# Kernel tuning notes

Hardware: AMD Instinct MI355X
Metric: run time of the kernel (lower is better)

The kernel has to match this reference:

```python
import jax, jax.numpy as jnp
import numpy as np

DIM = 128; PDIM = 32; WS = 16; HEADS = 4; NBLK = 2

def gelu(x):
    return jax.nn.gelu(x, approximate=False)  # torch default GELU (erf)

def conv2d(x, w, b=None, pad=0, groups=1):
    y = jax.lax.conv_general_dilated(x, w, (1, 1), [(pad, pad), (pad, pad)],
                                     feature_group_count=groups,
                                     dimension_numbers=('NCHW', 'OIHW', 'NCHW'))
    if b is not None:
        y = y + b[None, :, None, None]
    return y

def layernorm_cf(x, w, b, eps=1e-6):
    # channels_first LayerNorm over C per (b,h,w)
    m = x.mean(axis=1, keepdims=True)
    v = ((x - m) ** 2).mean(axis=1, keepdims=True)
    return (x - m) / jnp.sqrt(v + eps) * w[None, :, None, None] + b[None, :, None, None]

def conv_ffn(x, w1, b1, dw, dwb, w2, b2):
    y = gelu(conv2d(x, w1, b1, 0))
    y = gelu(conv2d(y, dw, dwb, 1, groups=y.shape[1])) + y
    return conv2d(y, w2, b2, 0)

def conv_attention(x, lk, pw1, pb1, pw2, pb2):
    # ConvolutionalAttention (training branch math, non-inplace)
    B, C, H, W = x.shape
    x1, x2 = x[:, :PDIM], x[:, PDIM:]
    # dwc_proj: global avg pool -> 1x1 -> GELU -> 1x1 (pure matmuls on pooled vec)
    v = x1.mean(axis=(2, 3))                              # [B, PDIM]
    h = gelu(v @ pw1[:, :, 0, 0].T + pb1)                 # [B, PDIM//2]
    dk = (h @ pw2[:, :, 0, 0].T + pb2).reshape(B * PDIM, 1, 3, 3)
    # per-sample dynamic depthwise conv via groups = B*PDIM
    dyn = conv2d(x1.reshape(1, B * PDIM, H, W), dk, None, 1,
                 groups=B * PDIM).reshape(B, PDIM, H, W)
    x1 = conv2d(x1, lk, None, lk.shape[-1] // 2) + dyn
    return jnp.concatenate([x1, x2], axis=1)

def window_attention(x, qkv_w, qkv_b, out_w, out_b, table):
    B, C, H, W = x.shape  # H,W divisible by WS -> pad_to_win is a no-op
    hd, wd = H // WS, W // WS
    c = C // HEADS
    qkv = conv2d(x, qkv_w, qkv_b, 0)                      # [B, 3C, H, W]
    qkv = qkv.reshape(B, 3, HEADS, c, hd, WS, wd, WS)
    qkv = qkv.transpose(1, 0, 4, 6, 2, 5, 7, 3).reshape(3, B * hd * wd, HEADS, WS * WS, c)
    q, k, v = qkv[0], qkv[1], qkv[2]
    S = WS * WS
    idx = jnp.arange(S); qh = idx // WS; qw = idx % WS
    rel = (qh[None, :] - qh[:, None] + WS - 1) * (2 * WS - 1) + (qw[None, :] - qw[:, None] + WS - 1)
    bias = table[:, rel]                                  # [HEADS, S, S]
    scores = jnp.einsum('nhqc,nhkc->nhqk', q, k) * (c ** -0.5) + bias[None]
    attn = jax.nn.softmax(scores, axis=-1)
    o = jnp.einsum('nhqk,nhkc->nhqc', attn, v)
    o = o.reshape(B, hd, wd, HEADS, WS, WS, c).transpose(0, 3, 6, 1, 4, 2, 5).reshape(B, C, H, W)
    return conv2d(o, out_w, out_b, 0)

def forward(x, plk_filter, ln_proj_w, ln_proj_b, proj_w1, proj_b1, proj_dw, proj_dwb,
            proj_w2, proj_b2, ln_attn_w, ln_attn_b, qkv_w, qkv_b, attn_out_w, attn_out_b,
            rpe_table, ffn_w1, ffn_b1, ffn_dw, ffn_dwb, ffn_w2, ffn_b2,
            pk_w1, pk_b1, pk_w2, pk_b2, pk_aggr_w, pk_aggr_b,
            ln_out_w, ln_out_b, co_w, co_b):
    skip = x
    x = layernorm_cf(x, ln_proj_w, ln_proj_b)
    x = conv_ffn(x, proj_w1, proj_b1, proj_dw, proj_dwb, proj_w2, proj_b2)
    x = x + window_attention(layernorm_cf(x, ln_attn_w, ln_attn_b),
                             qkv_w, qkv_b, attn_out_w, attn_out_b, rpe_table)
    for i in range(NBLK):
        y = conv_ffn(x, ffn_w1[i], ffn_b1[i], ffn_dw[i], ffn_dwb[i], ffn_w2[i], ffn_b2[i])
        y = conv_attention(y, plk_filter, pk_w1[i], pk_b1[i], pk_w2[i], pk_b2[i])
        y = conv2d(y, pk_aggr_w[i], pk_aggr_b[i], 0)
        x = x + y
    x = conv2d(layernorm_cf(x, ln_out_w, ln_out_b), co_w, co_b, 1)
    return x + skip

def setup_inputs() -> dict:
    key = jax.random.key(0)
    ks = iter(jax.random.split(key, 64))
    def rn(shape, s=0.02):
        return jax.random.normal(next(ks), shape, jnp.float32) * s
    d = DIM; e = 2 * d
    return dict(
        x=jax.random.normal(next(ks), (4, d, 192, 192), jnp.float32),
        plk_filter=rn((PDIM, PDIM, 13, 13), 0.05),
        ln_proj_w=jnp.ones((d,), jnp.float32), ln_proj_b=jnp.zeros((d,), jnp.float32),
        proj_w1=rn((e, d, 1, 1)), proj_b1=rn((e,)),
        proj_dw=rn((e, 1, 3, 3), 0.1), proj_dwb=rn((e,)),
        proj_w2=rn((d, e, 1, 1)), proj_b2=rn((d,)),
        ln_attn_w=jnp.ones((d,), jnp.float32), ln_attn_b=jnp.zeros((d,), jnp.float32),
        qkv_w=rn((3 * d, d, 1, 1)), qkv_b=rn((3 * d,)),
        attn_out_w=rn((d, d, 1, 1)), attn_out_b=rn((d,)),
        rpe_table=rn((HEADS, (2 * WS - 1) ** 2), 0.001),
        ffn_w1=rn((NBLK, e, d, 1, 1)), ffn_b1=rn((NBLK, e)),
        ffn_dw=rn((NBLK, e, 1, 3, 3), 0.1), ffn_dwb=rn((NBLK, e)),
        ffn_w2=rn((NBLK, d, e, 1, 1)), ffn_b2=rn((NBLK, d)),
        pk_w1=rn((NBLK, PDIM // 2, PDIM, 1, 1)), pk_b1=rn((NBLK, PDIM // 2)),
        pk_w2=rn((NBLK, PDIM * 9, PDIM // 2, 1, 1), 0.01), pk_b2=rn((NBLK, PDIM * 9), 0.01),
        pk_aggr_w=rn((NBLK, d, d, 1, 1)), pk_aggr_b=rn((NBLK, d)),
        ln_out_w=jnp.ones((d,), jnp.float32), ln_out_b=jnp.zeros((d,), jnp.float32),
        co_w=rn((d, d, 3, 3), 0.05), co_b=rn((d,)),
    )

def reference(x, plk_filter, ln_proj_w, ln_proj_b, proj_w1, proj_b1, proj_dw, proj_dwb,
              proj_w2, proj_b2, ln_attn_w, ln_attn_b, qkv_w, qkv_b, attn_out_w, attn_out_b,
              rpe_table, ffn_w1, ffn_b1, ffn_dw, ffn_dwb, ffn_w2, ffn_b2,
              pk_w1, pk_b1, pk_w2, pk_b2, pk_aggr_w, pk_aggr_b,
              ln_out_w, ln_out_b, co_w, co_b):
    return forward(x, plk_filter, ln_proj_w, ln_proj_b, proj_w1, proj_b1, proj_dw, proj_dwb,
                   proj_w2, proj_b2, ln_attn_w, ln_attn_b, qkv_w, qkv_b, attn_out_w, attn_out_b,
                   rpe_table, ffn_w1, ffn_b1, ffn_dw, ffn_dwb, ffn_w2, ffn_b2,
                   pk_w1, pk_b1, pk_w2, pk_b2, pk_aggr_w, pk_aggr_b,
                   ln_out_w, ln_out_b, co_w, co_b)
```

## Files before the change

kernel.cpp:

```cpp
#include <hip/hip_runtime.h>
#include <cmath>

#define HWD 192
#define PIX (HWD*HWD)
#define BB  4
#define CCH 128

using short8 = __attribute__((ext_vector_type(8))) short;
using f32x4  = __attribute__((ext_vector_type(4))) float;

__device__ __forceinline__ float gelu_f(float x) {
    return 0.5f * x * (1.0f + erff(x * 0.70710678118654752f));
}
__device__ __forceinline__ unsigned short f2bf(float f) {
    unsigned int u = __float_as_uint(f);
    u += 0x7fff + ((u >> 16) & 1);
    return (unsigned short)(u >> 16);
}
__device__ __forceinline__ float bf2f(unsigned short s) {
    return __uint_as_float((unsigned int)s << 16);
}
__device__ __forceinline__ unsigned pack2bf(float a, float b) {
    return (unsigned)f2bf(a) | ((unsigned)f2bf(b) << 16);
}

__global__ __launch_bounds__(256) void ln_t_kernel(const float* __restrict__ in,
        const float* __restrict__ w, const float* __restrict__ b,
        unsigned short* __restrict__ outT)
{
    int t = blockIdx.x * 256 + threadIdx.x;
    int bi = t / PIX;
    int p  = t - bi*PIX;
    const float* base = in + (size_t)bi * CCH * PIX + p;
    float v[CCH];
    float s = 0.f;
    #pragma unroll
    for (int c=0;c<CCH;++c) { v[c] = base[(size_t)c*PIX]; s += v[c]; }
    float m = s * (1.f/128.f);
    float q = 0.f;
    #pragma unroll
    for (int c=0;c<CCH;++c) { float d = v[c]-m; q += d*d; }
    float iv = rsqrtf(q*(1.f/128.f) + 1e-6f);
    unsigned short* ob = outT + ((size_t)bi * PIX + p) * 128;
    #pragma unroll
    for (int qq=0; qq<16; ++qq) {
        unsigned short e[8];
        #pragma unroll
        for (int j=0;j<8;++j) {
            int c = qq*8 + j;
            e[j] = f2bf((v[c]-m)*iv*w[c] + b[c]);
        }
        *(uint4*)&ob[qq*8] = *(uint4*)e;
    }
}

__global__ __launch_bounds__(256) void t32_kernel(const unsigned short* __restrict__ in,
    unsigned short* __restrict__ outT)
{
    int t = blockIdx.x * 256 + threadIdx.x;
    int bi = t / PIX;
    int p  = t - bi*PIX;
    const unsigned short* base = in + (size_t)bi * CCH * PIX + p;
    unsigned short e[32];
    #pragma unroll
    for (int c=0;c<32;++c) e[c] = base[(size_t)c*PIX];
    unsigned short* ob = outT + ((size_t)bi * PIX + p) * 32;
    #pragma unroll
    for (int q=0;q<4;++q) *(uint4*)&ob[q*8] = *(uint4*)&e[q*8];
}

template<typename TIN, bool TRANSIN, bool DOGELU, bool DORES, bool OBF>
__global__ __launch_bounds__(256) void conv1x1_mfma_kernel(
    const TIN* __restrict__ in,
    const unsigned short* __restrict__ wq,
    const float* __restrict__ bias,
    const float* __restrict__ res,
    void* __restrict__ outv,
    int Cin)
{
    constexpr int CIP = 72;
    __shared__ unsigned short XL[128*CIP];
    const int Cout = gridDim.y * 128;
    const int px0 = blockIdx.x * 128;
    const int co0 = blockIdx.y * 128;
    const size_t bi = blockIdx.z;
    in  += bi * (size_t)Cin * PIX;
    if (DORES) res += bi * (size_t)Cout * PIX;
    float* outf = (float*)outv + bi * (size_t)Cout * PIX;
    unsigned short* outb = (unsigned short*)outv + bi * (size_t)Cout * PIX;
    const int tid = threadIdx.x;
    const int lane = tid & 63, wid = tid >> 6;
    const int wco = (wid >> 1) * 64;
    const int wpx = (wid & 1) * 64;
    const int l15 = lane & 15, l4 = lane >> 4;

    f32x4 acc[4][4];
    #pragma unroll
    for (int i=0;i<4;++i)
        #pragma unroll
        for (int j=0;j<4;++j) acc[i][j] = (f32x4){0.f,0.f,0.f,0.f};

    for (int k0 = 0; k0 < Cin; k0 += 64) {
        __syncthreads();
        if constexpr (TRANSIN) {
            #pragma unroll
            for (int it = 0; it < 4; ++it) {
                int idx = tid + it*256;
                int q = idx & 7, px = idx >> 3;
                const uint4 v = *(const uint4*)((const unsigned short*)in
                                + ((size_t)(px0 + px))*128 + k0 + q*8);
                *(uint4*)&XL[px*CIP + q*8] = v;
            }
        } else {
            #pragma unroll
            for (int it = 0; it < 2; ++it) {
                int idx = tid + it*256;
                int c2  = idx & 31;
                int s   = idx >> 5;
                const TIN* g0 = in + (size_t)(k0 + c2*2    )*PIX + px0 + s*8;
                const TIN* g1 = in + (size_t)(k0 + c2*2 + 1)*PIX + px0 + s*8;
                unsigned short a8[8], b8[8];
                if constexpr (sizeof(TIN) == 2) {
                    *(uint4*)a8 = *(const uint4*)g0;
                    *(uint4*)b8 = *(const uint4*)g1;
                } else {
                    const float4 f0 = *(const float4*)g0;
                    const float4 f1 = *(const float4*)(g0+4);
                    const float4 f2 = *(const float4*)g1;
                    const float4 f3 = *(const float4*)(g1+4);
                    a8[0]=f2bf(f0.x); a8[1]=f2bf(f0.y); a8[2]=f2bf(f0.z); a8[3]=f2bf(f0.w);
                    a8[4]=f2bf(f1.x); a8[5]=f2bf(f1.y); a8[6]=f2bf(f1.z); a8[7]=f2bf(f1.w);
                    b8[0]=f2bf(f2.x); b8[1]=f2bf(f2.y); b8[2]=f2bf(f2.z); b8[3]=f2bf(f2.w);
                    b8[4]=f2bf(f3.x); b8[5]=f2bf(f3.y); b8[6]=f2bf(f3.z); b8[7]=f2bf(f3.w);
                }
                #pragma unroll
                for (int j=0;j<8;++j) {
                    unsigned pk = (unsigned)a8[j] | ((unsigned)b8[j] << 16);
                    *(unsigned*)&XL[(s*8+j)*CIP + c2*2] = pk;
                }
            }
        }
        __syncthreads();
        #pragma unroll
        for (int ks = 0; ks < 2; ++ks) {
            short8 a[4];
            #pragma unroll
            for (int mt=0; mt<4; ++mt) {
                int co = co0 + wco + mt*16 + l15;
                a[mt] = *(const short8*)(wq + (size_t)co*Cin + k0 + ks*32 + l4*8);
            }
            #pragma unroll
            for (int nt=0; nt<4; ++nt) {
                const short8 b = *(const short8*)&XL[(wpx + nt*16 + l15)*CIP + ks*32 + l4*8];
                #pragma unroll
                for (int mt=0; mt<4; ++mt)
                    acc[mt][nt] = __builtin_amdgcn_mfma_f32_16x16x32_bf16(a[mt], b, acc[mt][nt], 0, 0, 0);
            }
        }
    }
    #pragma unroll
    for (int mt=0; mt<4; ++mt) {
        #pragma unroll
        for (int r=0; r<4; ++r) {
            int co = co0 + wco + mt*16 + l4*4 + r;
            float bs = bias[co];
            #pragma unroll
            for (int nt=0; nt<4; ++nt) {
                int px = px0 + wpx + nt*16 + l15;
                float v = acc[mt][nt][r] + bs;
                if (DOGELU) v = gelu_f(v);
                size_t o = (size_t)co*PIX + px;
                if (DORES) v += res[o];
                if (OBF) outb[o] = f2bf(v);
                else     outf[o] = v;
            }
        }
    }
}

__global__ __launch_bounds__(256) void conv3x3_mfma_kernel(
    const unsigned short* __restrict__ inT,
    const unsigned short* __restrict__ wq,
    const float* __restrict__ bias, const float* __restrict__ skip,
    float* __restrict__ out)
{
    constexpr int CIP = 72;
    __shared__ unsigned short XL[4*66*CIP];
    const int x0 = blockIdx.x * 64;
    const int y0 = blockIdx.y * 2;
    const int bi = blockIdx.z;
    const int tid = threadIdx.x;
    const int lane = tid & 63, wid = tid >> 6;
    const int wco = (wid >> 1) * 64;
    const int wrow = wid & 1;
    const int l15 = lane & 15, l4 = lane >> 4;
    const unsigned short* inb = inT + (size_t)bi * PIX * 128;

    f32x4 acc[4][4];
    #pragma unroll
    for (int i=0;i<4;++i)
        #pragma unroll
        for (int j=0;j<4;++j) acc[i][j] = (f32x4){0.f,0.f,0.f,0.f};

    for (int ci0 = 0; ci0 < 128; ci0 += 64) {
        __syncthreads();
        #pragma unroll
        for (int it = 0; it < 9; ++it) {
            int idx = tid + it*256;
            if (idx < 2112) {
                int P = idx >> 3;
                int q = idx & 7;
                int row = P / 66;
                int x = P - row*66;
                int gy = y0 - 1 + row, gx = x0 - 1 + x;
                uint4 v = {0u,0u,0u,0u};
                if ((unsigned)gy < (unsigned)HWD && (unsigned)gx < (unsigned)HWD)
                    v = *(const uint4*)&inb[((size_t)gy*HWD + gx)*128 + ci0 + q*8];
                *(uint4*)&XL[P*CIP + q*8] = v;
            }
        }
        __syncthreads();
        #pragma unroll
        for (int dy=0; dy<3; ++dy) {
            #pragma unroll
            for (int dx=0; dx<3; ++dx) {
                const int rl = wrow + dy;
                #pragma unroll
                for (int ks=0; ks<2; ++ks) {
                    short8 a[4];
                    #pragma unroll
                    for (int mt=0; mt<4; ++mt) {
                        int co = wco + mt*16 + l15;
                        a[mt] = *(const short8*)(wq + ((size_t)co*9 + dy*3+dx)*128 + ci0 + ks*32 + l4*8);
                    }
                    #pragma unroll
                    for (int nt=0; nt<4; ++nt) {
                        const int xl = nt*16 + l15 + dx;
                        const short8 b = *(const short8*)&XL[(rl*66 + xl)*CIP + ks*32 + l4*8];
                        #pragma unroll
                        for (int mt=0; mt<4; ++mt)
                            acc[mt][nt] = __builtin_amdgcn_mfma_f32_16x16x32_bf16(a[mt], b, acc[mt][nt], 0, 0, 0);
                    }
                }
            }
        }
    }
    const int gy = y0 + wrow;
    #pragma unroll
    for (int mt=0; mt<4; ++mt) {
        #pragma unroll
        for (int r=0; r<4; ++r) {
            int co = wco + mt*16 + l4*4 + r;
            float bs = bias[co];
            #pragma unroll
            for (int nt=0; nt<4; ++nt) {
                int gx = x0 + nt*16 + l15;
                size_t o = ((size_t)bi*CCH + co)*PIX + (size_t)gy*HWD + gx;
                out[o] = acc[mt][nt][r] + bs + skip[o];
            }
        }
    }
}

__global__ __launch_bounds__(256) void conv13_mfma_kernel(
    const unsigned short* __restrict__ YT,
    const unsigned short* __restrict__ wq,
    const float* __restrict__ dk,
    unsigned short* __restrict__ outL)
{
    __shared__ unsigned short XL[16*76*32];
    const int x0 = blockIdx.x * 64;
    const int y0 = blockIdx.y * 4;
    const int bi = blockIdx.z;
    const int tid = threadIdx.x;
    const int lane = tid & 63, wr = tid >> 6;
    const int l15 = lane & 15, l4 = lane >> 4;
    const unsigned short* inT = YT + (size_t)bi * PIX * 32;

    #pragma unroll 1
    for (int it = 0; it < 19; ++it) {
        int idx = tid + it*256;
        int P = idx >> 2;
        int q = idx & 3;
        int row = P / 76;
        int x   = P - row*76;
        int gy = y0 - 6 + row, gx = x0 - 6 + x;
        uint4 v = {0u,0u,0u,0u};
        if ((unsigned)gy < (unsigned)HWD && (unsigned)gx < (unsigned)HWD)
            v = *(const uint4*)&inT[((size_t)gy*HWD + gx)*32 + q*8];
        *(uint4*)&XL[P*32 + ((q*8) ^ ((P&3)<<3))] = v;
    }
    __syncthreads();

    f32x4 acc[2][4];
    #pragma unroll
    for (int i=0;i<2;++i)
        #pragma unroll
        for (int j=0;j<4;++j) acc[i][j] = (f32x4){0.f,0.f,0.f,0.f};

    #pragma unroll 1
    for (int dy=0; dy<13; ++dy) {
        const unsigned short* wrow = wq + (size_t)dy*13*1024;
        #pragma unroll
        for (int dx=0; dx<13; ++dx) {
            const short8 a0 = *(const short8*)(wrow + dx*1024 + l15*32 + l4*8);
            const short8 a1 = *(const short8*)(wrow + dx*1024 + (16+l15)*32 + l4*8);
            #pragma unroll
            for (int nt=0; nt<4; ++nt) {
                const int P = (wr + dy)*76 + nt*16 + l15 + dx;
                const short8 b = *(const short8*)&XL[P*32 + ((l4*8) ^ ((P&3)<<3))];
                acc[0][nt] = __builtin_amdgcn_mfma_f32_16x16x32_bf16(a0, b, acc[0][nt], 0, 0, 0);
                acc[1][nt] = __builtin_amdgcn_mfma_f32_16x16x32_bf16(a1, b, acc[1][nt], 0, 0, 0);
            }
        }
    }
    const int gy = y0 + wr;
    #pragma unroll
    for (int mt=0; mt<2; ++mt) {
        #pragma unroll
        for (int r=0; r<4; ++r) {
            const int co = mt*16 + l4*4 + r;
            const float* dkk = dk + (bi*32 + co)*9;
            float k0=dkk[0],k1=dkk[1],k2=dkk[2],k3=dkk[3],k4=dkk[4],
                  k5=dkk[5],k6=dkk[6],k7=dkk[7],k8=dkk[8];
            #pragma unroll
            for (int nt=0; nt<4; ++nt) {
                const int px = nt*16 + l15;
                float dsum = 0.f;
                #pragma unroll
                for (int e=0; e<9; ++e) {
                    int ey = e/3, ex = e - ey*3;
                    int P = (wr+5+ey)*76 + px+5+ex;
                    float pv = bf2f(XL[P*32 + (co ^ ((P&3)<<3))]);
                    float kk = (e==0?k0:e==1?k1:e==2?k2:e==3?k3:e==4?k4:e==5?k5:e==6?k6:e==7?k7:k8);
                    dsum += pv * kk;
                }
                float v = acc[mt][nt][r] + dsum;
                outL[((size_t)bi*CCH + co)*PIX + (size_t)gy*HWD + x0 + px] = f2bf(v);
            }
        }
    }
}

__global__ __launch_bounds__(256) void dw3x3_bf_kernel(const unsigned short* __restrict__ in,
    const float* __restrict__ w, const float* __restrict__ b,
    unsigned short* __restrict__ out)
{
    int t = blockIdx.x*256 + threadIdx.x;
    int pc = t / (PIX/4);
    int p4 = (t - pc*(PIX/4)) * 4;
    int c = pc & 255;
    int y = p4 / HWD, x0 = p4 - y*HWD;
    const unsigned short* ib = in + (size_t)pc * PIX;
    float wk[9];
    #pragma unroll
    for (int e=0;e<9;++e) wk[e] = w[c*9+e];
    float bc = b[c];
    float a0=bc,a1=bc,a2=bc,a3=bc;
    #pragma unroll
    for (int ky=0;ky<3;++ky) {
        int yy = y + ky - 1;
        if ((unsigned)yy < (unsigned)HWD) {
            const unsigned short* row = ib + (size_t)yy*HWD;
            float v[6];
            #pragma unroll
            for (int d=0;d<6;++d) {
                int xx = x0 + d - 1;
                v[d] = ((unsigned)xx < (unsigned)HWD) ? bf2f(row[xx]) : 0.f;
            }
            a0 += v[0]*wk[ky*3+0] + v[1]*wk[ky*3+1] + v[2]*wk[ky*3+2];
            a1 += v[1]*wk[ky*3+0] + v[2]*wk[ky*3+1] + v[3]*wk[ky*3+2];
            a2 += v[2]*wk[ky*3+0] + v[3]*wk[ky*3+1] + v[4]*wk[ky*3+2];
            a3 += v[3]*wk[ky*3+0] + v[4]*wk[ky*3+1] + v[5]*wk[ky*3+2];
        }
    }
    const unsigned short* cen = ib + (size_t)y*HWD + x0;
    unsigned short r0 = f2bf(gelu_f(a0) + bf2f(cen[0]));
    unsigned short r1 = f2bf(gelu_f(a1) + bf2f(cen[1]));
    unsigned short r2 = f2bf(gelu_f(a2) + bf2f(cen[2]));
    unsigned short r3 = f2bf(gelu_f(a3) + bf2f(cen[3]));
    uint2 pk;
    pk.x = (unsigned)r0 | ((unsigned)r1 << 16);
    pk.y = (unsigned)r2 | ((unsigned)r3 << 16);
    *(uint2*)(out + (size_t)pc*PIX + p4) = pk;
}

__global__ __launch_bounds__(256) void attn_mfma_kernel(
    const unsigned short* __restrict__ qkv,
    const float* __restrict__ table,
    unsigned short* __restrict__ o)
{
    __shared__ unsigned short KL[256*44];
    __shared__ unsigned short VL[32*264];
    __shared__ unsigned short PL[4*16*40];
    __shared__ float BT[961];
    __shared__ unsigned short OL[64*33];
    const int win = blockIdx.x, head = blockIdx.y;
    const int bi2 = blockIdx.z;
    const int wy = win/12, wx = win - wy*12;
    qkv += (size_t)bi2 * 384 * PIX;
    o   += (size_t)bi2 * CCH * PIX;
    const unsigned short* qb = qkv + (size_t)(head*32) * PIX;
    const unsigned short* kb = qkv + (size_t)(128 + head*32) * PIX;
    const unsigned short* vb = qkv + (size_t)(256 + head*32) * PIX;
    const int tid = threadIdx.x;

    #pragma unroll
    for (int it = 0; it < 4; ++it) {
        int idx = tid + it*256;
        int c = idx & 31, seg = idx >> 5;
        int k0 = seg*8;
        int sp = ((wy<<4) + (k0>>4))*HWD + (wx<<4) + (k0&15);
        *(uint4*)&VL[c*264 + k0] = *(const uint4*)&vb[(size_t)c*PIX + sp];
    }
    #pragma unroll
    for (int it = 0; it < 4; ++it) {
        int idx = tid + it*256;
        int c = idx & 31, seg = idx >> 5;
        int k0 = seg*8;
        int sp = ((wy<<4) + (k0>>4))*HWD + (wx<<4) + (k0&15);
        unsigned short e[8];
        *(uint4*)e = *(const uint4*)&kb[(size_t)c*PIX + sp];
        #pragma unroll
        for (int j=0;j<8;++j) KL[(k0+j)*44 + c] = e[j];
    }
    for (int i = tid; i < 961; i += 256) BT[i] = table[head*961 + i];
    __syncthreads();

    const int lane = tid & 63, w = tid >> 6;
    const int l15 = lane & 15, l4 = lane >> 4;
    const float scale = 0.17677669529663687f;
    unsigned short* PLw = &PL[w*16*40];

    #pragma unroll 1
    for (int qc = 0; qc < 4; ++qc) {
        const int qi = qc*64 + w*16 + l15;
        const int iy = qi >> 4, ix = qi & 15;
        const int spq = ((wy<<4) + iy)*HWD + (wx<<4) + ix;

        short8 qf;
        #pragma unroll
        for (int j=0;j<8;++j) qf[j] = (short)qb[(size_t)(l4*8+j)*PIX + spq];

        f32x4 s[16];
        #pragma unroll
        for (int nt=0; nt<16; ++nt) {
            const short8 a = *(const short8*)&KL[(nt*16 + l15)*44 + l4*8];
            s[nt] = __builtin_amdgcn_mfma_f32_16x16x32_bf16(a, qf, (f32x4){0.f,0.f,0.f,0.f}, 0, 0, 0);
        }

        float m = -1e30f;
        #pragma unroll
        for (int nt=0; nt<16; ++nt) {
            #pragma unroll
            for (int r=0; r<4; ++r) {
                int k = nt*16 + l4*4 + r;
                float bv = BT[((k>>4) - iy + 15)*31 + ((k&15) - ix + 15)];
                float v = s[nt][r]*scale + bv;
                s[nt][r] = v;
                m = fmaxf(m, v);
            }
        }
        m = fmaxf(m, __shfl_xor(m, 16, 64));
        m = fmaxf(m, __shfl_xor(m, 32, 64));
        float l = 0.f;
        #pragma unroll
        for (int nt=0; nt<16; ++nt) {
            #pragma unroll
            for (int r=0; r<4; ++r) {
                float p = __expf(s[nt][r] - m);
                s[nt][r] = p;
                l += p;
            }
        }
        l += __shfl_xor(l, 16, 64);
        l += __shfl_xor(l, 32, 64);

        f32x4 o0 = (f32x4){0.f,0.f,0.f,0.f}, o1 = (f32x4){0.f,0.f,0.f,0.f};
        #pragma unroll
        for (int kt=0; kt<8; ++kt) {
            #pragma unroll
            for (int h=0; h<2; ++h) {
                int nt = kt*2 + h;
                *(unsigned*)&PLw[l15*40 + h*16 + l4*4]     = pack2bf(s[nt][0], s[nt][1]);
                *(unsigned*)&PLw[l15*40 + h*16 + l4*4 + 2] = pack2bf(s[nt][2], s[nt][3]);
            }
            const short8 pa = *(const short8*)&PLw[l15*40 + l4*8];
            const short8 v0 = *(const short8*)&VL[l15*264 + kt*32 + l4*8];
            const short8 v1 = *(const short8*)&VL[(16+l15)*264 + kt*32 + l4*8];
            o0 = __builtin_amdgcn_mfma_f32_16x16x32_bf16(pa, v0, o0, 0, 0, 0);
            o1 = __builtin_amdgcn_mfma_f32_16x16x32_bf16(pa, v1, o1, 0, 0, 0);
        }

        #pragma unroll
        for (int r=0; r<4; ++r) {
            float lr = __shfl(l, l4*4 + r, 64);
            float inv = 1.f / lr;
            OL[(w*16 + l4*4 + r)*33 + l15]      = f2bf(o0[r]*inv);
            OL[(w*16 + l4*4 + r)*33 + 16 + l15] = f2bf(o1[r]*inv);
        }
        __syncthreads();

        const int d = tid >> 3, seg = tid & 7;
        const int q0l = seg*8;
        const int qi0 = qc*64 + q0l;
        const int sp0 = ((wy<<4) + (qi0>>4))*HWD + (wx<<4) + (qi0 & 15);
        unsigned short tmp[8];
        #pragma unroll
        for (int j=0;j<8;++j) tmp[j] = OL[(q0l+j)*33 + d];
        *(uint4*)&o[(size_t)(head*32 + d)*PIX + sp0] = *(uint4*)tmp;
        __syncthreads();
    }
}

__global__ __launch_bounds__(256) void meanpool_kernel(const unsigned short* __restrict__ in,
    float* __restrict__ v)
{
    int bc = blockIdx.x;
    int bi = bc >> 5, c = bc & 31;
    const unsigned short* base = in + ((size_t)bi*CCH + c) * PIX;
    float s = 0.f;
    for (int i = threadIdx.x; i < PIX/4; i += 256) {
        const uint2 t4 = ((const uint2*)base)[i];
        s += bf2f((unsigned short)(t4.x & 0xffff)) + bf2f((unsigned short)(t4.x >> 16))
           + bf2f((unsigned short)(t4.y & 0xffff)) + bf2f((unsigned short)(t4.y >> 16));
    }
    #pragma unroll
    for (int off=32; off>0; off>>=1) s += __shfl_down(s, off, 64);
    __shared__ float red[4];
    if ((threadIdx.x & 63) == 0) red[threadIdx.x >> 6] = s;
    __syncthreads();
    if (threadIdx.x == 0) v[bc] = (red[0]+red[1]+red[2]+red[3]) * (1.f/PIX);
}

__global__ __launch_bounds__(256) void mlp_kernel(const float* __restrict__ v,
    const float* __restrict__ pw1, const float* __restrict__ pb1,
    const float* __restrict__ pw2, const float* __restrict__ pb2,
    float* __restrict__ dk)
{
    __shared__ float h[64];
    int tid = threadIdx.x;
    if (tid < 64) {
        int bi = tid >> 4, m = tid & 15;
        float s = pb1[m];
        for (int c=0;c<32;++c) s += v[bi*32+c]*pw1[m*32+c];
        h[tid] = gelu_f(s);
    }
    __syncthreads();
    for (int idx = tid; idx < BB*288; idx += 256) {
        int bi = idx / 288, j = idx - bi*288;
        float s = pb2[j];
        for (int m=0;m<16;++m) s += h[bi*16+m]*pw2[j*16+m];
        dk[idx] = s;
    }
}

__global__ __launch_bounds__(256) void wcast_kernel(const float* __restrict__ w,
    unsigned short* __restrict__ wq, int n)
{
    int idx = blockIdx.x*256 + threadIdx.x;
    if (idx < n) wq[idx] = f2bf(w[idx]);
}

__global__ __launch_bounds__(256) void w3cast_kernel(const float* __restrict__ w,
    unsigned short* __restrict__ wq)
{
    int idx = blockIdx.x*256 + threadIdx.x;
    if (idx >= 128*128*9) return;
    int co = idx / (128*9);
    int rem = idx - co*128*9;
    int ci = rem / 9;
    int tap = rem - ci*9;
    wq[((size_t)co*9 + tap)*128 + ci] = f2bf(w[idx]);
}

__global__ __launch_bounds__(256) void w13cast_kernel(const float* __restrict__ w,
    unsigned short* __restrict__ wq)
{
    int idx = blockIdx.x*256 + threadIdx.x;
    if (idx >= 32*32*169) return;
    int co = idx / (32*169);
    int rem = idx - co*32*169;
    int ci = rem / 169;
    int tap = rem - ci*169;
    wq[((size_t)tap*32 + co)*32 + ci] = f2bf(w[idx]);
}

extern "C" void kernel_launch(void* const* d_in, const int* in_sizes, int n_in,
                              void* d_out, int out_size, void* d_ws, size_t ws_size,
                              hipStream_t stream) {
    (void)in_sizes; (void)n_in; (void)out_size;
    const float* x_in      = (const float*)d_in[0];
    const float* plk       = (const float*)d_in[1];
    const float* ln_proj_w = (const float*)d_in[2];
    const float* ln_proj_b = (const float*)d_in[3];
    const float* proj_w1   = (const float*)d_in[4];
    const float* proj_b1   = (const float*)d_in[5];
    const float* proj_dw   = (const float*)d_in[6];
    const float* proj_dwb  = (const float*)d_in[7];
    const float* proj_w2   = (const float*)d_in[8];
    const float* proj_b2   = (const float*)d_in[9];
    const float* ln_attn_w = (const float*)d_in[10];
    const float* ln_attn_b = (const float*)d_in[11];
    const float* qkv_w     = (const float*)d_in[12];
    const float* qkv_b     = (const float*)d_in[13];
    const float* attn_ow   = (const float*)d_in[14];
    const float* attn_ob   = (const float*)d_in[15];
    const float* rpe       = (const float*)d_in[16];
    const float* ffn_w1    = (const float*)d_in[17];
    const float* ffn_b1    = (const float*)d_in[18];
    const float* ffn_dw    = (const float*)d_in[19];
    const float* ffn_dwb   = (const float*)d_in[20];
    const float* ffn_w2    = (const float*)d_in[21];
    const float* ffn_b2    = (const float*)d_in[22];
    const float* pk_w1     = (const float*)d_in[23];
    const float* pk_b1     = (const float*)d_in[24];
    const float* pk_w2     = (const float*)d_in[25];
    const float* pk_b2     = (const float*)d_in[26];
    const float* aggr_w    = (const float*)d_in[27];
    const float* aggr_b    = (const float*)d_in[28];
    const float* ln_out_w  = (const float*)d_in[29];
    const float* ln_out_b  = (const float*)d_in[30];
    const float* co_w      = (const float*)d_in[31];
    const float* co_b      = (const float*)d_in[32];
    float* out = (float*)d_out;

    const size_t N1b = (size_t)CCH * PIX;
    const size_t RBsz = (size_t)BB * N1b;
    const size_t LNYw = RBsz / 2;
    const size_t YTw  = (size_t)BB*PIX*32/2;
    const size_t TAILw = 256 + 1152 + 307712/2 + 64;
    const size_t need_half = RBsz + LNYw + RBsz   + YTw + TAILw;
    const size_t need_full = RBsz + LNYw + 2*RBsz + YTw + TAILw;
    if (ws_size < need_half * sizeof(float)) return;
    const bool full = ws_size >= need_full * sizeof(float);
    const size_t Ew = full ? 2*RBsz : RBsz;

    float* ws  = (float*)d_ws;
    float* RB  = ws;
    unsigned short* LNY  = (unsigned short*)(RB + RBsz);
    unsigned short* EP   = (unsigned short*)(RB + RBsz + LNYw);
    unsigned short* YT   = (unsigned short*)(RB + RBsz + LNYw + Ew);
    float* VB  = (float*)(RB + RBsz + LNYw + Ew + YTw);
    float* DK  = VB + 256;
    unsigned short* Q0  = (unsigned short*)(DK + 1152);
    unsigned short* qPW1 = Q0;
    unsigned short* qPW2 = qPW1 + 32768;
    unsigned short* qQKV = qPW2 + 32768;
    unsigned short* qAT  = qQKV + 49152;
    unsigned short* qF1  = qAT  + 16384;
    unsigned short* qF2  = qF1  + 65536;
    unsigned short* qAG  = qF2  + 65536;
    unsigned short* qW3  = qAG  + 32768;
    unsigned short* qW13 = qW3  + 147456;

    const int NZ = full ? BB : 2;
    const int NH = full ? 1 : 2;
    unsigned short* E1 = EP;
    unsigned short* E2 = EP + (size_t)NZ*256*PIX;
    unsigned short* QKV = EP;
    unsigned short* XT  = EP;

    dim3 blk(256);

    wcast_kernel<<<128, blk, 0, stream>>>(proj_w1, qPW1, 32768);
    wcast_kernel<<<128, blk, 0, stream>>>(proj_w2, qPW2, 32768);
    wcast_kernel<<<192, blk, 0, stream>>>(qkv_w, qQKV, 49152);
    wcast_kernel<<<64,  blk, 0, stream>>>(attn_ow, qAT, 16384);
    wcast_kernel<<<256, blk, 0, stream>>>(ffn_w1, qF1, 65536);
    wcast_kernel<<<256, blk, 0, stream>>>(ffn_w2, qF2, 65536);
    wcast_kernel<<<128, blk, 0, stream>>>(aggr_w, qAG, 32768);
    w3cast_kernel<<<576, blk, 0, stream>>>(co_w, qW3);
    w13cast_kernel<<<676, blk, 0, stream>>>(plk, qW13);

    ln_t_kernel<<<576, blk, 0, stream>>>(x_in, ln_proj_w, ln_proj_b, LNY);
    for (int h=0; h<NH; ++h) {
        conv1x1_mfma_kernel<unsigned short,true,true,false,true><<<dim3(288,2,NZ), blk, 0, stream>>>(
            LNY + (size_t)h*NZ*N1b, qPW1, proj_b1, nullptr, E1, 128);
        dw3x3_bf_kernel<<<NZ*9216, blk, 0, stream>>>(E1, proj_dw, proj_dwb, E2);
        conv1x1_mfma_kernel<unsigned short,false,false,false,false><<<dim3(288,1,NZ), blk, 0, stream>>>(
            E2, qPW2, proj_b2, nullptr, RB + (size_t)h*NZ*N1b, 256);
    }

    ln_t_kernel<<<576, blk, 0, stream>>>(RB, ln_attn_w, ln_attn_b, LNY);
    for (int h=0; h<NH; ++h) {
        conv1x1_mfma_kernel<unsigned short,true,false,false,true><<<dim3(288,3,NZ), blk, 0, stream>>>(
            LNY + (size_t)h*NZ*N1b, qQKV, qkv_b, nullptr, QKV, 128);
        attn_mfma_kernel<<<dim3(144,4,NZ), blk, 0, stream>>>(QKV, rpe, LNY + (size_t)h*NZ*N1b);
    }
    conv1x1_mfma_kernel<unsigned short,false,false,true,false><<<dim3(288,1,BB), blk, 0, stream>>>(
        LNY, qAT, attn_ob, RB, RB, 128);

    for (int i=0;i<2;++i) {
        const float* fb1 = ffn_b1 + (size_t)i*256;
        const float* fdw = ffn_dw + (size_t)i*256*9;
        const float* fdb = ffn_dwb + (size_t)i*256;
        const float* fb2 = ffn_b2 + (size_t)i*128;
        const float* w1i = pk_w1 + (size_t)i*16*32;
        const float* b1i = pk_b1 + (size_t)i*16;
        const float* w2i = pk_w2 + (size_t)i*288*16;
        const float* b2i = pk_b2 + (size_t)i*288;
        const float* abi = aggr_b + (size_t)i*128;

        for (int h=0; h<NH; ++h) {
            conv1x1_mfma_kernel<float,false,true,false,true><<<dim3(288,2,NZ), blk, 0, stream>>>(
                RB + (size_t)h*NZ*N1b, qF1 + (size_t)i*32768, fb1, nullptr, E1, 128);
            dw3x3_bf_kernel<<<NZ*9216, blk, 0, stream>>>(E1, fdw, fdb, E2);
            conv1x1_mfma_kernel<unsigned short,false,false,false,true><<<dim3(288,1,NZ), blk, 0, stream>>>(
                E2, qF2 + (size_t)i*32768, fb2, nullptr, LNY + (size_t)h*NZ*N1b, 256);
        }
        t32_kernel<<<576, blk, 0, stream>>>(LNY, YT);
        meanpool_kernel<<<BB*32, blk, 0, stream>>>(LNY, VB);
        mlp_kernel<<<1, blk, 0, stream>>>(VB, w1i, b1i, w2i, b2i, DK);
        conv13_mfma_kernel<<<dim3(3,48,BB), blk, 0, stream>>>(YT, qW13, DK, LNY);
        conv1x1_mfma_kernel<unsigned short,false,false,true,false><<<dim3(288,1,BB), blk, 0, stream>>>(
            LNY, qAG + (size_t)i*16384, abi, RB, RB, 128);
    }

    ln_t_kernel<<<576, blk, 0, stream>>>(RB, ln_out_w, ln_out_b, XT);
    conv3x3_mfma_kernel<<<dim3(3,96,BB), blk, 0, stream>>>(XT, qW3, co_b, x_in, out);
}
```

Baseline: 1.501 ms.

## Coalesce attention Q loads, per-wave output staging, bf16 bias table, fuse weight casts

Measured after the change: 1.541 ms. 2.7% more time.

```diff
diff --git a/kernel.cpp b/kernel.cpp
--- a/kernel.cpp
+++ b/kernel.cpp
@@ -390,11 +390,12 @@
     const float* __restrict__ table,
     unsigned short* __restrict__ o)
 {
-    __shared__ unsigned short KL[256*44];
+    __shared__ unsigned short KL[256*40];
     __shared__ unsigned short VL[32*264];
+    __shared__ unsigned short QL[4*16*40];
     __shared__ unsigned short PL[4*16*40];
-    __shared__ float BT[961];
-    __shared__ unsigned short OL[64*33];
+    __shared__ unsigned short OL[4*16*33];
+    __shared__ unsigned short BTh[961];
     const int win = blockIdx.x, head = blockIdx.y;
     const int bi2 = blockIdx.z;
     const int wy = win/12, wx = win - wy*12;
@@ -422,41 +423,47 @@
         unsigned short e[8];
         *(uint4*)e = *(const uint4*)&kb[(size_t)c*PIX + sp];
         #pragma unroll
-        for (int j=0;j<8;++j) KL[(k0+j)*44 + c] = e[j];
-    }
-    for (int i = tid; i < 961; i += 256) BT[i] = table[head*961 + i];
+        for (int j=0;j<8;++j) KL[(k0+j)*40 + c] = e[j];
+    }
+    for (int i = tid; i < 961; i += 256) BTh[i] = f2bf(table[head*961 + i]);
     __syncthreads();
 
     const int lane = tid & 63, w = tid >> 6;
     const int l15 = lane & 15, l4 = lane >> 4;
+    const int c32 = lane & 31, sg = lane >> 5;
     const float scale = 0.17677669529663687f;
+    unsigned short* QLw = &QL[w*16*40];
     unsigned short* PLw = &PL[w*16*40];
+    unsigned short* OLw = &OL[w*16*33];
 
     #pragma unroll 1
     for (int qc = 0; qc < 4; ++qc) {
-        const int qi = qc*64 + w*16 + l15;
-        const int iy = qi >> 4, ix = qi & 15;
-        const int spq = ((wy<<4) + iy)*HWD + (wx<<4) + ix;
-
-        short8 qf;
-        #pragma unroll
-        for (int j=0;j<8;++j) qf[j] = (short)qb[(size_t)(l4*8+j)*PIX + spq];
+        const int prow = (qc<<2) + w;
+        const int rowsp = ((wy<<4) + prow)*HWD + (wx<<4);
+
+        {
+            unsigned short e[8];
+            *(uint4*)e = *(const uint4*)&qb[(size_t)c32*PIX + rowsp + sg*8];
+            #pragma unroll
+            for (int j=0;j<8;++j) QLw[(sg*8+j)*40 + c32] = e[j];
+        }
+        const short8 qf = *(const short8*)&QLw[l15*40 + l4*8];
 
         f32x4 s[16];
         #pragma unroll
         for (int nt=0; nt<16; ++nt) {
-            const short8 a = *(const short8*)&KL[(nt*16 + l15)*44 + l4*8];
+            const short8 a = *(const short8*)&KL[(nt*16 + l15)*40 + l4*8];
             s[nt] = __builtin_amdgcn_mfma_f32_16x16x32_bf16(a, qf, (f32x4){0.f,0.f,0.f,0.f}, 0, 0, 0);
         }
 
+        const int bidx0 = (15 - prow)*31 + (15 - l15) + l4*4;
         float m = -1e30f;
         #pragma unroll
         for (int nt=0; nt<16; ++nt) {
+            const int bb = bidx0 + nt*31;
             #pragma unroll
             for (int r=0; r<4; ++r) {
-                int k = nt*16 + l4*4 + r;
-                float bv = BT[((k>>4) - iy + 15)*31 + ((k&15) - ix + 15)];
-                float v = s[nt][r]*scale + bv;
+                float v = s[nt][r]*scale + bf2f(BTh[bb + r]);
                 s[nt][r] = v;
                 m = fmaxf(m, v);
             }
@@ -496,20 +503,13 @@
         for (int r=0; r<4; ++r) {
             float lr = __shfl(l, l4*4 + r, 64);
             float inv = 1.f / lr;
-            OL[(w*16 + l4*4 + r)*33 + l15]      = f2bf(o0[r]*inv);
-            OL[(w*16 + l4*4 + r)*33 + 16 + l15] = f2bf(o1[r]*inv);
-        }
-        __syncthreads();
-
-        const int d = tid >> 3, seg = tid & 7;
-        const int q0l = seg*8;
-        const int qi0 = qc*64 + q0l;
-        const int sp0 = ((wy<<4) + (qi0>>4))*HWD + (wx<<4) + (qi0 & 15);
+            OLw[(l4*4+r)*33 + l15]      = f2bf(o0[r]*inv);
+            OLw[(l4*4+r)*33 + 16 + l15] = f2bf(o1[r]*inv);
+        }
         unsigned short tmp[8];
         #pragma unroll
-        for (int j=0;j<8;++j) tmp[j] = OL[(q0l+j)*33 + d];
-        *(uint4*)&o[(size_t)(head*32 + d)*PIX + sp0] = *(uint4*)tmp;
-        __syncthreads();
+        for (int j=0;j<8;++j) tmp[j] = OLw[(sg*8+j)*33 + c32];
+        *(uint4*)&o[(size_t)(head*32 + c32)*PIX + rowsp + sg*8] = *(uint4*)tmp;
     }
 }
 
@@ -555,35 +555,44 @@
     }
 }
 
-__global__ __launch_bounds__(256) void wcast_kernel(const float* __restrict__ w,
-    unsigned short* __restrict__ wq, int n)
+__global__ __launch_bounds__(256) void wprep_kernel(
+    const float* __restrict__ proj_w1, const float* __restrict__ proj_w2,
+    const float* __restrict__ qkv_w,   const float* __restrict__ attn_ow,
+    const float* __restrict__ ffn_w1,  const float* __restrict__ ffn_w2,
+    const float* __restrict__ aggr_w,  const float* __restrict__ co_w,
+    const float* __restrict__ plk,     unsigned short* __restrict__ Q0)
 {
     int idx = blockIdx.x*256 + threadIdx.x;
-    if (idx < n) wq[idx] = f2bf(w[idx]);
-}
-
-__global__ __launch_bounds__(256) void w3cast_kernel(const float* __restrict__ w,
-    unsigned short* __restrict__ wq)
-{
-    int idx = blockIdx.x*256 + threadIdx.x;
-    if (idx >= 128*128*9) return;
-    int co = idx / (128*9);
-    int rem = idx - co*128*9;
-    int ci = rem / 9;
-    int tap = rem - ci*9;
-    wq[((size_t)co*9 + tap)*128 + ci] = f2bf(w[idx]);
-}
-
-__global__ __launch_bounds__(256) void w13cast_kernel(const float* __restrict__ w,
-    unsigned short* __restrict__ wq)
-{
-    int idx = blockIdx.x*256 + threadIdx.x;
-    if (idx >= 32*32*169) return;
-    int co = idx / (32*169);
-    int rem = idx - co*32*169;
-    int ci = rem / 169;
-    int tap = rem - ci*169;
-    wq[((size_t)tap*32 + co)*32 + ci] = f2bf(w[idx]);
+    if (idx < 32768) { Q0[idx] = f2bf(proj_w1[idx]); return; }
+    idx -= 32768;
+    if (idx < 32768) { Q0[32768 + idx] = f2bf(proj_w2[idx]); return; }
+    idx -= 32768;
+    if (idx < 49152) { Q0[65536 + idx] = f2bf(qkv_w[idx]); return; }
+    idx -= 49152;
+    if (idx < 16384) { Q0[114688 + idx] = f2bf(attn_ow[idx]); return; }
+    idx -= 16384;
+    if (idx < 65536) { Q0[131072 + idx] = f2bf(ffn_w1[idx]); return; }
+    idx -= 65536;
+    if (idx < 65536) { Q0[196608 + idx] = f2bf(ffn_w2[idx]); return; }
+    idx -= 65536;
+    if (idx < 32768) { Q0[262144 + idx] = f2bf(aggr_w[idx]); return; }
+    idx -= 32768;
+    if (idx < 147456) {
+        int co = idx / (128*9);
+        int rem = idx - co*128*9;
+        int ci = rem / 9;
+        int tap = rem - ci*9;
+        Q0[294912 + ((size_t)co*9 + tap)*128 + ci] = f2bf(co_w[idx]);
+        return;
+    }
+    idx -= 147456;
+    if (idx < 173056) {
+        int co = idx / (32*169);
+        int rem = idx - co*32*169;
+        int ci = rem / 169;
+        int tap = rem - ci*169;
+        Q0[442368 + ((size_t)tap*32 + co)*32 + ci] = f2bf(plk[idx]);
+    }
 }
 
 extern "C" void kernel_launch(void* const* d_in, const int* in_sizes, int n_in,
@@ -629,7 +638,8 @@
     const size_t RBsz = (size_t)BB * N1b;
     const size_t LNYw = RBsz / 2;
     const size_t YTw  = (size_t)BB*PIX*32/2;
-    const size_t TAILw = 256 + 1152 + 307712/2 + 64;
+    const size_t QTOT = 615424;
+    const size_t TAILw = 256 + 1152 + QTOT/2 + 64;
     const size_t need_half = RBsz + LNYw + RBsz   + YTw + TAILw;
     const size_t need_full = RBsz + LNYw + 2*RBsz + YTw + TAILw;
     if (ws_size < need_half * sizeof(float)) return;
@@ -663,15 +673,8 @@
 
     dim3 blk(256);
 
-    wcast_kernel<<<128, blk, 0, stream>>>(proj_w1, qPW1, 32768);
-    wcast_kernel<<<128, blk, 0, stream>>>(proj_w2, qPW2, 32768);
-    wcast_kernel<<<192, blk, 0, stream>>>(qkv_w, qQKV, 49152);
-    wcast_kernel<<<64,  blk, 0, stream>>>(attn_ow, qAT, 16384);
-    wcast_kernel<<<256, blk, 0, stream>>>(ffn_w1, qF1, 65536);
-    wcast_kernel<<<256, blk, 0, stream>>>(ffn_w2, qF2, 65536);
-    wcast_kernel<<<128, blk, 0, stream>>>(aggr_w, qAG, 32768);
-    w3cast_kernel<<<576, blk, 0, stream>>>(co_w, qW3);
-    w13cast_kernel<<<676, blk, 0, stream>>>(plk, qW13);
+    wprep_kernel<<<(615424+255)/256, blk, 0, stream>>>(
+        proj_w1, proj_w2, qkv_w, attn_ow, ffn_w1, ffn_w2, aggr_w, co_w, plk, Q0);
 
     ln_t_kernel<<<576, blk, 0, stream>>>(x_in, ln_proj_w, ln_proj_b, LNY);
     for (int h=0; h<NH; ++h) {
```
